# Kernel optimization log

Measured on AMD Instinct MI355X. Metric: run time of the kernel, lower is better.

The kernel has to match this reference:

```python
import jax, jax.numpy as jnp
import numpy as np

L, D, H, DFF, V, NB = 8, 1024, 16, 4096, 50257, 2048
HD = D // H
B, T = 2, 2048
EPS = 1e-5


def setup_inputs() -> dict:
    key = jax.random.key(0)
    ks = jax.random.split(key, 10)
    s = 0.02
    return {
        "x": jax.random.randint(ks[0], (B, T), 0, V),
        "W_emb": jax.random.normal(ks[1], (V, D), jnp.float32) * s,  # tied tok_emb / out_head
        "pos_emb": jax.random.normal(ks[2], (NB, D), jnp.float32) * s,
        "Wq": jax.random.normal(ks[3], (L, D, D), jnp.float32) * s,
        "Wk": jax.random.normal(ks[4], (L, D, D), jnp.float32) * s,
        "Wv": jax.random.normal(ks[5], (L, D, D), jnp.float32) * s,
        "Wo": jax.random.normal(ks[6], (L, D, D), jnp.float32) * s,
        "bo": jnp.zeros((L, D), jnp.float32),
        "n1_scale": jnp.ones((L, D), jnp.float32),
        "n1_shift": jnp.zeros((L, D), jnp.float32),
        "n2_scale": jnp.ones((L, D), jnp.float32),
        "n2_shift": jnp.zeros((L, D), jnp.float32),
        "W1": jax.random.normal(ks[7], (L, DFF, D), jnp.float32) * s,
        "b1": jnp.zeros((L, DFF), jnp.float32),
        "W2": jax.random.normal(ks[8], (L, D, DFF), jnp.float32) * s,
        "b2": jnp.zeros((L, D), jnp.float32),
        "f_scale": jnp.ones((D,), jnp.float32),
        "f_shift": jnp.zeros((D,), jnp.float32),
    }


def layernorm(x, scale, shift):
    # Matches custom LayerNorm: uses sample std (ddof=1) and (std + eps) in denominator
    mean = jnp.mean(x, axis=-1, keepdims=True)
    std = jnp.std(x, axis=-1, keepdims=True, ddof=1)
    return scale * ((x - mean) / (std + EPS)) + shift


def gelu(x):
    c = jnp.sqrt(jnp.asarray(2.0 / jnp.pi, x.dtype))
    return 0.5 * x * (1.0 + jnp.tanh(c * (x + 0.044715 * x * x * x)))


def reference(x, W_emb, pos_emb, Wq, Wk, Wv, Wo, bo,
              n1_scale, n1_shift, n2_scale, n2_shift,
              W1, b1, W2, b2, f_scale, f_shift):
    b, t = x.shape
    h = W_emb[x] + pos_emb[:t]  # [B,T,D]
    causal = jnp.triu(jnp.ones((t, t), dtype=bool), 1)  # True above diagonal => masked
    scale = jnp.sqrt(jnp.asarray(HD, h.dtype))
    neg_inf = jnp.asarray(-jnp.inf, h.dtype)
    for l in range(L):
        xn = layernorm(h, n1_scale[l], n1_shift[l])
        q = (xn @ Wq[l].T).reshape(b, t, H, HD).transpose(0, 2, 1, 3)  # [B,H,T,hd]
        k = (xn @ Wk[l].T).reshape(b, t, H, HD).transpose(0, 2, 1, 3)
        v = (xn @ Wv[l].T).reshape(b, t, H, HD).transpose(0, 2, 1, 3)
        scores = jnp.einsum('bhqd,bhkd->bhqk', q, k)
        scores = jnp.where(causal, neg_inf, scores) / scale  # mask then scale, as in source
        aw = jax.nn.softmax(scores, axis=-1)
        ctx = jnp.einsum('bhqk,bhkd->bhqd', aw, v)
        ctx = ctx.transpose(0, 2, 1, 3).reshape(b, t, D)
        h = h + (ctx @ Wo[l].T + bo[l])
        xn2 = layernorm(h, n2_scale[l], n2_shift[l])
        h = h + (gelu(xn2 @ W1[l].T + b1[l]) @ W2[l].T + b2[l])
    h = layernorm(h, f_scale, f_shift)
    logits = h[:, -1:, :] @ W_emb.T  # last-token logits [B,1,V] (targets=None path)
    return logits
```

## Files before the change

### kernel.cpp

```cpp
#include <hip/hip_runtime.h>
#include <math.h>

#define L_   8
#define D_   1024
#define H_   16
#define HD_  64
#define DFF_ 4096
#define V_   50257
#define T_   2048
#define B_   2
#define M_   (B_*T_)

typedef __attribute__((ext_vector_type(8))) short short8;
typedef __attribute__((ext_vector_type(4))) float f4;
typedef __attribute__((ext_vector_type(4))) unsigned short us4;

#define GLOAD16(gp, lp) \
  __builtin_amdgcn_global_load_lds((__attribute__((address_space(1))) void*)(gp), \
                                   (__attribute__((address_space(3))) void*)(lp), 16, 0, 0)

__device__ __forceinline__ unsigned short f2bf(float f) {
  union { float f; unsigned u; } c; c.f = f;
  return (unsigned short)((c.u + 0x7fffu + ((c.u >> 16) & 1u)) >> 16);
}

__global__ __launch_bounds__(256) void cvt_kernel(const float* __restrict__ s,
                                                  unsigned short* __restrict__ d, int n) {
  int i = (blockIdx.x * 256 + threadIdx.x) * 4;
  const int stride = gridDim.x * 256 * 4;
  for (; i < n; i += stride) {
    f4 f = *(const f4*)(s + i);
    us4 o;
    o.x = f2bf(f.x); o.y = f2bf(f.y); o.z = f2bf(f.z); o.w = f2bf(f.w);
    *(us4*)(d + i) = o;
  }
}

__global__ __launch_bounds__(256) void embed_kernel(const int* __restrict__ x,
    const float* __restrict__ wemb, const float* __restrict__ pos, float* __restrict__ h) {
  const int m = blockIdx.x;
  const int t = m & (T_ - 1);
  const int idx = x[m];
  const int d = threadIdx.x * 4;
  f4 a = *(const f4*)(wemb + (size_t)idx * D_ + d);
  f4 b = *(const f4*)(pos + (size_t)t * D_ + d);
  a = a + b;
  *(f4*)(h + (size_t)m * D_ + d) = a;
}

__global__ __launch_bounds__(256) void ln_kernel(const float* __restrict__ h,
    const float* __restrict__ sc, const float* __restrict__ sh,
    unsigned short* __restrict__ out) {
  const int row = blockIdx.x, tid = threadIdx.x;
  f4 x = *(const f4*)(h + (size_t)row * D_ + tid * 4);
  float s1 = x.x + x.y + x.z + x.w;
  float s2 = x.x * x.x + x.y * x.y + x.z * x.z + x.w * x.w;
#pragma unroll
  for (int off = 32; off > 0; off >>= 1) {
    s1 += __shfl_down(s1, off);
    s2 += __shfl_down(s2, off);
  }
  __shared__ float r1[4], r2[4];
  if ((tid & 63) == 0) { r1[tid >> 6] = s1; r2[tid >> 6] = s2; }
  __syncthreads();
  float t1 = r1[0] + r1[1] + r1[2] + r1[3];
  float t2 = r2[0] + r2[1] + r2[2] + r2[3];
  float mean = t1 * (1.0f / D_);
  float var = fmaxf((t2 - t1 * mean) * (1.0f / (D_ - 1)), 0.0f);
  float inv = 1.0f / (sqrtf(var) + 1e-5f);
  f4 s = *(const f4*)(sc + tid * 4);
  f4 b = *(const f4*)(sh + tid * 4);
  us4 o;
  o.x = f2bf(s.x * ((x.x - mean) * inv) + b.x);
  o.y = f2bf(s.y * ((x.y - mean) * inv) + b.y);
  o.z = f2bf(s.z * ((x.z - mean) * inv) + b.z);
  o.w = f2bf(s.w * ((x.w - mean) * inv) + b.w);
  *(us4*)(out + (size_t)row * D_ + tid * 4) = o;
}

__global__ __launch_bounds__(256) void ln_final_kernel(const float* __restrict__ h,
    const float* __restrict__ sc, const float* __restrict__ sh, float* __restrict__ out) {
  const int b = blockIdx.x, tid = threadIdx.x;
  const int row = b * T_ + (T_ - 1);
  f4 x = *(const f4*)(h + (size_t)row * D_ + tid * 4);
  float s1 = x.x + x.y + x.z + x.w;
  float s2 = x.x * x.x + x.y * x.y + x.z * x.z + x.w * x.w;
#pragma unroll
  for (int off = 32; off > 0; off >>= 1) {
    s1 += __shfl_down(s1, off);
    s2 += __shfl_down(s2, off);
  }
  __shared__ float r1[4], r2[4];
  if ((tid & 63) == 0) { r1[tid >> 6] = s1; r2[tid >> 6] = s2; }
  __syncthreads();
  float t1 = r1[0] + r1[1] + r1[2] + r1[3];
  float t2 = r2[0] + r2[1] + r2[2] + r2[3];
  float mean = t1 * (1.0f / D_);
  float var = fmaxf((t2 - t1 * mean) * (1.0f / (D_ - 1)), 0.0f);
  float inv = 1.0f / (sqrtf(var) + 1e-5f);
  f4 s = *(const f4*)(sc + tid * 4);
  f4 bb = *(const f4*)(sh + tid * 4);
  f4 o;
  o.x = s.x * ((x.x - mean) * inv) + bb.x;
  o.y = s.y * ((x.y - mean) * inv) + bb.y;
  o.z = s.z * ((x.z - mean) * inv) + bb.z;
  o.w = s.w * ((x.w - mean) * inv) + bb.w;
  *(f4*)(out + (size_t)b * D_ + tid * 4) = o;
}

#define EP_QKV 0
#define EP_RES 1
#define EP_GELU 2

template <int MODE>
__global__ __launch_bounds__(256) void gemm_kernel(
    const unsigned short* __restrict__ A,
    const unsigned short* __restrict__ Bq,
    const unsigned short* __restrict__ Bk,
    const unsigned short* __restrict__ Bv,
    const float* __restrict__ bias,
    float* __restrict__ hres,
    unsigned short* __restrict__ out0,
    unsigned short* __restrict__ out1,
    unsigned short* __restrict__ out2,
    int N, int K) {
  __shared__ __attribute__((aligned(16))) unsigned short As[128 * 32];
  __shared__ __attribute__((aligned(16))) unsigned short Bs[128 * 32];
  const int tid = threadIdx.x;
  const int wv = tid >> 6, lane = tid & 63;
  const int quad = lane >> 4, l16 = lane & 15;
  const int bm0 = blockIdx.x * 128;
  int bn0;
  const unsigned short* Bw;
  unsigned short* qout = out0;
  if (MODE == EP_QKV) {
    int sel = blockIdx.y >> 3;
    bn0 = (blockIdx.y & 7) * 128;
    Bw = (sel == 0) ? Bq : ((sel == 1) ? Bk : Bv);
    qout = (sel == 0) ? out0 : ((sel == 1) ? out1 : out2);
  } else {
    bn0 = blockIdx.y * 128;
    Bw = Bq;
  }
  const int wm = (wv & 1) * 64, wn = (wv >> 1) * 64;

  f4 acc[4][4] = {};

  for (int k0 = 0; k0 < K; k0 += 32) {
#pragma unroll
    for (int i = 0; i < 2; i++) {
      int c = i * 256 + tid;
      int row = c >> 2;
      int c4 = (c & 3) ^ (row & 3);
      GLOAD16(A + (size_t)(bm0 + row) * K + k0 + c4 * 8,
              (char*)As + (i * 256 + wv * 64) * 16);
      GLOAD16(Bw + (size_t)(bn0 + row) * K + k0 + c4 * 8,
              (char*)Bs + (i * 256 + wv * 64) * 16);
    }
    __syncthreads();
    short8 af[4], bfr[4];
#pragma unroll
    for (int mt = 0; mt < 4; mt++) {
      int row = wm + mt * 16 + l16;
      af[mt] = *(const short8*)(As + row * 32 + ((quad ^ (row & 3)) * 8));
    }
#pragma unroll
    for (int nt = 0; nt < 4; nt++) {
      int row = wn + nt * 16 + l16;
      bfr[nt] = *(const short8*)(Bs + row * 32 + ((quad ^ (row & 3)) * 8));
    }
#pragma unroll
    for (int mt = 0; mt < 4; mt++)
#pragma unroll
      for (int nt = 0; nt < 4; nt++)
        acc[mt][nt] = __builtin_amdgcn_mfma_f32_16x16x32_bf16(af[mt], bfr[nt], acc[mt][nt], 0, 0, 0);
    __syncthreads();
  }

#pragma unroll
  for (int mt = 0; mt < 4; mt++) {
#pragma unroll
    for (int nt = 0; nt < 4; nt++) {
#pragma unroll
      for (int r = 0; r < 4; r++) {
        int gm = bm0 + wm + mt * 16 + quad * 4 + r;
        int gn = bn0 + wn + nt * 16 + l16;
        float val = acc[mt][nt][r];
        if (MODE == EP_QKV) {
          int b = gm >> 11, t = gm & (T_ - 1);
          int hh = gn >> 6, hd = gn & 63;
          qout[(size_t)((b * H_ + hh) * T_ + t) * HD_ + hd] = f2bf(val);
        } else if (MODE == EP_RES) {
          size_t idx = (size_t)gm * D_ + gn;
          hres[idx] += val + bias[gn];
        } else {
          float xg = val + bias[gn];
          float z = 0.7978845608028654f * (xg + 0.044715f * xg * xg * xg);
          float e = __expf(2.0f * z);
          float th = 1.0f - 2.0f / (e + 1.0f);
          out0[(size_t)gm * DFF_ + gn] = f2bf(0.5f * xg * (1.0f + th));
        }
      }
    }
  }
}

__global__ __launch_bounds__(256) void vtrans_kernel(const unsigned short* __restrict__ v,
                                                     unsigned short* __restrict__ vt) {
  __shared__ __attribute__((aligned(16))) unsigned short tile[64 * 72];
  const int tid = threadIdx.x;
  const int t0 = blockIdx.x * 64;
  const size_t bh = (size_t)(blockIdx.z * H_ + blockIdx.y);
  const unsigned short* vp = v + bh * T_ * HD_;
#pragma unroll
  for (int i = 0; i < 2; i++) {
    int c = i * 256 + tid;
    int row = c >> 3, c8 = c & 7;
    *(short8*)(tile + row * 72 + c8 * 8) =
        *(const short8*)(vp + (size_t)(t0 + row) * HD_ + c8 * 8);
  }
  __syncthreads();
  unsigned short* op = vt + bh * (size_t)HD_ * T_;
#pragma unroll
  for (int i = 0; i < 2; i++) {
    int c = i * 256 + tid;
    int drow = c >> 3, c8 = c & 7;
    short8 o;
#pragma unroll
    for (int j = 0; j < 8; j++) o[j] = (short)tile[(c8 * 8 + j) * 72 + drow];
    *(short8*)(op + (size_t)drow * T_ + t0 + c8 * 8) = o;
  }
}

__global__ __launch_bounds__(256) void attn_kernel(
    const unsigned short* __restrict__ q,
    const unsigned short* __restrict__ k,
    const unsigned short* __restrict__ vt,
    unsigned short* __restrict__ ctx) {
  __shared__ __attribute__((aligned(16))) unsigned short Ks[64 * 64];
  __shared__ __attribute__((aligned(16))) unsigned short Vs[64 * 64];
  __shared__ __attribute__((aligned(16))) unsigned short Ps[4][16 * 88];
  const int tid = threadIdx.x;
  const int wv = tid >> 6, lane = tid & 63;
  const int quad = lane >> 4, l16 = lane & 15;
  const int qt = blockIdx.x, hh = blockIdx.y, b = blockIdx.z;
  const size_t bh = (size_t)(b * H_ + hh);
  const unsigned short* qp = q + bh * T_ * HD_;
  const unsigned short* kp = k + bh * T_ * HD_;
  const unsigned short* vp = vt + bh * (size_t)HD_ * T_;

  const int qrow = qt * 64 + wv * 16 + l16;
  const short8 qf0 = *(const short8*)(qp + (size_t)qrow * HD_ + quad * 8);
  const short8 qf1 = *(const short8*)(qp + (size_t)qrow * HD_ + 32 + quad * 8);

  f4 of[4] = {};
  float mrow[4] = {-1e30f, -1e30f, -1e30f, -1e30f};
  float lrow[4] = {0.f, 0.f, 0.f, 0.f};
  unsigned short* pw = Ps[wv];

  const int nkt = qt + 1;
  for (int kt = 0; kt < nkt; kt++) {
    const int kb = kt * 64;
#pragma unroll
    for (int i = 0; i < 2; i++) {
      int c = i * 256 + tid;
      int row = c >> 3;
      int c8 = (c & 7) ^ (row & 7);
      GLOAD16(kp + (size_t)(kb + row) * HD_ + c8 * 8, (char*)Ks + (i * 256 + wv * 64) * 16);
      GLOAD16(vp + (size_t)row * T_ + kb + c8 * 8, (char*)Vs + (i * 256 + wv * 64) * 16);
    }
    __syncthreads();
    float sv[4][4];
#pragma unroll
    for (int nt = 0; nt < 4; nt++) {
      int row = nt * 16 + l16;
      int p0 = (quad ^ (row & 7)) * 8;
      int p1 = ((4 + quad) ^ (row & 7)) * 8;
      short8 kf0 = *(const short8*)(Ks + row * 64 + p0);
      short8 kf1 = *(const short8*)(Ks + row * 64 + p1);
      f4 z = {};
      z = __builtin_amdgcn_mfma_f32_16x16x32_bf16(qf0, kf0, z, 0, 0, 0);
      z = __builtin_amdgcn_mfma_f32_16x16x32_bf16(qf1, kf1, z, 0, 0, 0);
#pragma unroll
      for (int r = 0; r < 4; r++) {
        float s = z[r] * 0.125f;
        if (kt == qt) {
          int col = kb + nt * 16 + l16;
          int rowg = qt * 64 + wv * 16 + quad * 4 + r;
          if (col > rowg) s = -1e30f;
        }
        sv[nt][r] = s;
      }
    }
    float mnew[4], alpha[4];
#pragma unroll
    for (int r = 0; r < 4; r++) {
      float mx = fmaxf(fmaxf(sv[0][r], sv[1][r]), fmaxf(sv[2][r], sv[3][r]));
      mx = fmaxf(mx, __shfl_xor(mx, 1));
      mx = fmaxf(mx, __shfl_xor(mx, 2));
      mx = fmaxf(mx, __shfl_xor(mx, 4));
      mx = fmaxf(mx, __shfl_xor(mx, 8));
      mnew[r] = fmaxf(mrow[r], mx);
      alpha[r] = __expf(mrow[r] - mnew[r]);
      mrow[r] = mnew[r];
    }
    float pv[4][4];
#pragma unroll
    for (int nt = 0; nt < 4; nt++)
#pragma unroll
      for (int r = 0; r < 4; r++)
        pv[nt][r] = __expf(sv[nt][r] - mnew[r]);
#pragma unroll
    for (int r = 0; r < 4; r++) {
      float s = pv[0][r] + pv[1][r] + pv[2][r] + pv[3][r];
      s += __shfl_xor(s, 1);
      s += __shfl_xor(s, 2);
      s += __shfl_xor(s, 4);
      s += __shfl_xor(s, 8);
      lrow[r] = lrow[r] * alpha[r] + s;
    }
#pragma unroll
    for (int nt = 0; nt < 4; nt++) {
      of[nt][0] *= alpha[0];
      of[nt][1] *= alpha[1];
      of[nt][2] *= alpha[2];
      of[nt][3] *= alpha[3];
    }
#pragma unroll
    for (int nt = 0; nt < 4; nt++)
#pragma unroll
      for (int r = 0; r < 4; r++)
        pw[(quad * 4 + r) * 88 + nt * 16 + l16] = f2bf(pv[nt][r]);
    short8 pf0 = *(const short8*)(pw + l16 * 88 + quad * 8);
    short8 pf1 = *(const short8*)(pw + l16 * 88 + 32 + quad * 8);
#pragma unroll
    for (int nt = 0; nt < 4; nt++) {
      int row = nt * 16 + l16;
      int p0 = (quad ^ (row & 7)) * 8;
      int p1 = ((4 + quad) ^ (row & 7)) * 8;
      short8 vf0 = *(const short8*)(Vs + row * 64 + p0);
      short8 vf1 = *(const short8*)(Vs + row * 64 + p1);
      of[nt] = __builtin_amdgcn_mfma_f32_16x16x32_bf16(pf0, vf0, of[nt], 0, 0, 0);
      of[nt] = __builtin_amdgcn_mfma_f32_16x16x32_bf16(pf1, vf1, of[nt], 0, 0, 0);
    }
    __syncthreads();
  }
#pragma unroll
  for (int nt = 0; nt < 4; nt++) {
#pragma unroll
    for (int r = 0; r < 4; r++) {
      int rowg = qt * 64 + wv * 16 + quad * 4 + r;
      int dcol = hh * HD_ + nt * 16 + l16;
      ctx[(size_t)(b * T_ + rowg) * D_ + dcol] = f2bf(of[nt][r] / lrow[r]);
    }
  }
}

__global__ __launch_bounds__(256) void logits_kernel(const float* __restrict__ wemb,
    const float* __restrict__ hln, float* __restrict__ out) {
  const int tid = threadIdx.x;
  const int wv = tid >> 6, lane = tid & 63;
  const int rbase = blockIdx.x * 32 + wv * 8;
  f4 h0[4], h1[4];
#pragma unroll
  for (int j = 0; j < 4; j++) {
    h0[j] = *(const f4*)(hln + j * 256 + lane * 4);
    h1[j] = *(const f4*)(hln + D_ + j * 256 + lane * 4);
  }
#pragma unroll
  for (int i = 0; i < 8; i++) {
    int r = rbase + i;
    if (r >= V_) return;
    const float* wr = wemb + (size_t)r * D_;
    float a0 = 0.f, a1 = 0.f;
#pragma unroll
    for (int j = 0; j < 4; j++) {
      f4 w4 = *(const f4*)(wr + j * 256 + lane * 4);
      a0 += w4.x * h0[j].x + w4.y * h0[j].y + w4.z * h0[j].z + w4.w * h0[j].w;
      a1 += w4.x * h1[j].x + w4.y * h1[j].y + w4.z * h1[j].z + w4.w * h1[j].w;
    }
#pragma unroll
    for (int off = 32; off > 0; off >>= 1) {
      a0 += __shfl_down(a0, off);
      a1 += __shfl_down(a1, off);
    }
    if (lane == 0) {
      out[r] = a0;
      out[V_ + r] = a1;
    }
  }
}

extern "C" void kernel_launch(void* const* d_in, const int* in_sizes, int n_in,
                              void* d_out, int out_size, void* d_ws, size_t ws_size,
                              hipStream_t stream) {
  (void)in_sizes; (void)n_in; (void)out_size; (void)ws_size;
  const int*   x    = (const int*)  d_in[0];
  const float* Wemb = (const float*)d_in[1];
  const float* pos  = (const float*)d_in[2];
  const float* Wq   = (const float*)d_in[3];
  const float* Wk   = (const float*)d_in[4];
  const float* Wv   = (const float*)d_in[5];
  const float* Wo   = (const float*)d_in[6];
  const float* bo   = (const float*)d_in[7];
  const float* n1s  = (const float*)d_in[8];
  const float* n1b  = (const float*)d_in[9];
  const float* n2s  = (const float*)d_in[10];
  const float* n2b  = (const float*)d_in[11];
  const float* W1   = (const float*)d_in[12];
  const float* b1   = (const float*)d_in[13];
  const float* W2   = (const float*)d_in[14];
  const float* b2   = (const float*)d_in[15];
  const float* fsc  = (const float*)d_in[16];
  const float* fsh  = (const float*)d_in[17];
  float* out = (float*)d_out;

  char* p = (char*)d_ws;
  auto alloc = [&](size_t bytes) -> char* {
    char* r = p;
    p += (bytes + 255) & ~(size_t)255;
    return r;
  };
  unsigned short* wq_b = (unsigned short*)alloc((size_t)L_ * D_ * D_ * 2);
  unsigned short* wk_b = (unsigned short*)alloc((size_t)L_ * D_ * D_ * 2);
  unsigned short* wv_b = (unsigned short*)alloc((size_t)L_ * D_ * D_ * 2);
  unsigned short* wo_b = (unsigned short*)alloc((size_t)L_ * D_ * D_ * 2);
  unsigned short* w1_b = (unsigned short*)alloc((size_t)L_ * DFF_ * D_ * 2);
  unsigned short* w2_b = (unsigned short*)alloc((size_t)L_ * DFF_ * D_ * 2);
  float*          h    = (float*)alloc((size_t)M_ * D_ * 4);
  unsigned short* xn   = (unsigned short*)alloc((size_t)M_ * D_ * 2);
  unsigned short* qb   = (unsigned short*)alloc((size_t)M_ * D_ * 2);
  unsigned short* kb   = (unsigned short*)alloc((size_t)M_ * D_ * 2);
  unsigned short* vb   = (unsigned short*)alloc((size_t)M_ * D_ * 2);
  unsigned short* vtb  = (unsigned short*)alloc((size_t)M_ * D_ * 2);
  unsigned short* ctx  = (unsigned short*)alloc((size_t)M_ * D_ * 2);
  unsigned short* act  = (unsigned short*)alloc((size_t)M_ * DFF_ * 2);
  float*          hln  = (float*)alloc(2 * D_ * 4);

  cvt_kernel<<<2048, 256, 0, stream>>>(Wq, wq_b, L_ * D_ * D_);
  cvt_kernel<<<2048, 256, 0, stream>>>(Wk, wk_b, L_ * D_ * D_);
  cvt_kernel<<<2048, 256, 0, stream>>>(Wv, wv_b, L_ * D_ * D_);
  cvt_kernel<<<2048, 256, 0, stream>>>(Wo, wo_b, L_ * D_ * D_);
  cvt_kernel<<<2048, 256, 0, stream>>>(W1, w1_b, L_ * DFF_ * D_);
  cvt_kernel<<<2048, 256, 0, stream>>>(W2, w2_b, L_ * DFF_ * D_);
  embed_kernel<<<M_, 256, 0, stream>>>(x, Wemb, pos, h);

  for (int l = 0; l < L_; l++) {
    ln_kernel<<<M_, 256, 0, stream>>>(h, n1s + l * D_, n1b + l * D_, xn);
    gemm_kernel<EP_QKV><<<dim3(32, 24), 256, 0, stream>>>(
        xn, wq_b + (size_t)l * D_ * D_, wk_b + (size_t)l * D_ * D_,
        wv_b + (size_t)l * D_ * D_, nullptr, nullptr, qb, kb, vb, D_, D_);
    vtrans_kernel<<<dim3(32, H_, B_), 256, 0, stream>>>(vb, vtb);
    attn_kernel<<<dim3(32, H_, B_), 256, 0, stream>>>(qb, kb, vtb, ctx);
    gemm_kernel<EP_RES><<<dim3(32, 8), 256, 0, stream>>>(
        ctx, wo_b + (size_t)l * D_ * D_, nullptr, nullptr,
        bo + l * D_, h, nullptr, nullptr, nullptr, D_, D_);
    ln_kernel<<<M_, 256, 0, stream>>>(h, n2s + l * D_, n2b + l * D_, xn);
    gemm_kernel<EP_GELU><<<dim3(32, 32), 256, 0, stream>>>(
        xn, w1_b + (size_t)l * DFF_ * D_, nullptr, nullptr,
        b1 + l * DFF_, nullptr, act, nullptr, nullptr, DFF_, D_);
    gemm_kernel<EP_RES><<<dim3(32, 8), 256, 0, stream>>>(
        act, w2_b + (size_t)l * DFF_ * D_, nullptr, nullptr,
        b2 + l * D_, h, nullptr, nullptr, nullptr, D_, DFF_);
  }
  ln_final_kernel<<<2, 256, 0, stream>>>(h, fsc, fsh, hln);
  logits_kernel<<<(V_ + 31) / 32, 256, 0, stream>>>(Wemb, hln, out);
}
```

Measured before the change: 3.668 ms.

## Pair complementary causal query tiles per attention block to balance work

Each attention block now processes two query tiles, bx and 31-bx, sharing the same K/V tile loads from shared memory, so every block does roughly equal causal work and loaded K/V tiles are reused by both. The grid is halved to 16 blocks in x, and launch bounds request two blocks per CU. This aims to remove tail imbalance from triangular causal work and cut redundant K/V loads. The cost is more registers for two sets of accumulators and fewer total blocks (512), which may reduce occupancy or latency hiding.

Measured after the change: 3.263 ms. -11.0%, faster.

```diff
diff --git a/kernel.cpp b/kernel.cpp
--- a/kernel.cpp
+++ b/kernel.cpp
@@ -232,7 +232,74 @@
   }
 }
 
-__global__ __launch_bounds__(256) void attn_kernel(
+#define ATTN_STEP(QF0, QF1, OF, MR, LR, QT)                                        \
+  {                                                                                \
+    float sv[4][4];                                                                \
+    _Pragma("unroll") for (int nt = 0; nt < 4; nt++) {                             \
+      int row = nt * 16 + l16;                                                     \
+      int p0 = (quad ^ (row & 7)) * 8;                                             \
+      int p1 = ((4 + quad) ^ (row & 7)) * 8;                                       \
+      short8 kf0 = *(const short8*)(Ks + row * 64 + p0);                           \
+      short8 kf1 = *(const short8*)(Ks + row * 64 + p1);                           \
+      f4 z = {};                                                                   \
+      z = __builtin_amdgcn_mfma_f32_16x16x32_bf16(QF0, kf0, z, 0, 0, 0);           \
+      z = __builtin_amdgcn_mfma_f32_16x16x32_bf16(QF1, kf1, z, 0, 0, 0);           \
+      _Pragma("unroll") for (int r = 0; r < 4; r++) {                              \
+        float s = z[r] * 0.125f;                                                   \
+        if (kt == (QT)) {                                                          \
+          int col = kb + nt * 16 + l16;                                            \
+          int rowg = (QT) * 64 + wv * 16 + quad * 4 + r;                           \
+          if (col > rowg) s = -1e30f;                                              \
+        }                                                                          \
+        sv[nt][r] = s;                                                             \
+      }                                                                            \
+    }                                                                              \
+    float mnew[4], alpha[4];                                                       \
+    _Pragma("unroll") for (int r = 0; r < 4; r++) {                                \
+      float mx = fmaxf(fmaxf(sv[0][r], sv[1][r]), fmaxf(sv[2][r], sv[3][r]));      \
+      mx = fmaxf(mx, __shfl_xor(mx, 1));                                           \
+      mx = fmaxf(mx, __shfl_xor(mx, 2));                                           \
+      mx = fmaxf(mx, __shfl_xor(mx, 4));                                           \
+      mx = fmaxf(mx, __shfl_xor(mx, 8));                                           \
+      mnew[r] = fmaxf(MR[r], mx);                                                  \
+      alpha[r] = __expf(MR[r] - mnew[r]);                                          \
+      MR[r] = mnew[r];                                                             \
+    }                                                                              \
+    float pv[4][4];                                                                \
+    _Pragma("unroll") for (int nt = 0; nt < 4; nt++)                               \
+      _Pragma("unroll") for (int r = 0; r < 4; r++)                                \
+        pv[nt][r] = __expf(sv[nt][r] - mnew[r]);                                   \
+    _Pragma("unroll") for (int r = 0; r < 4; r++) {                                \
+      float s = pv[0][r] + pv[1][r] + pv[2][r] + pv[3][r];                         \
+      s += __shfl_xor(s, 1);                                                       \
+      s += __shfl_xor(s, 2);                                                       \
+      s += __shfl_xor(s, 4);                                                       \
+      s += __shfl_xor(s, 8);                                                       \
+      LR[r] = LR[r] * alpha[r] + s;                                                \
+    }                                                                              \
+    _Pragma("unroll") for (int nt = 0; nt < 4; nt++) {                             \
+      OF[nt][0] *= alpha[0];                                                       \
+      OF[nt][1] *= alpha[1];                                                       \
+      OF[nt][2] *= alpha[2];                                                       \
+      OF[nt][3] *= alpha[3];                                                       \
+    }                                                                              \
+    _Pragma("unroll") for (int nt = 0; nt < 4; nt++)                               \
+      _Pragma("unroll") for (int r = 0; r < 4; r++)                                \
+        pw[(quad * 4 + r) * 88 + nt * 16 + l16] = f2bf(pv[nt][r]);                 \
+    short8 pf0 = *(const short8*)(pw + l16 * 88 + quad * 8);                       \
+    short8 pf1 = *(const short8*)(pw + l16 * 88 + 32 + quad * 8);                  \
+    _Pragma("unroll") for (int nt = 0; nt < 4; nt++) {                             \
+      int row = nt * 16 + l16;                                                     \
+      int p0 = (quad ^ (row & 7)) * 8;                                             \
+      int p1 = ((4 + quad) ^ (row & 7)) * 8;                                       \
+      short8 vf0 = *(const short8*)(Vs + row * 64 + p0);                           \
+      short8 vf1 = *(const short8*)(Vs + row * 64 + p1);                           \
+      OF[nt] = __builtin_amdgcn_mfma_f32_16x16x32_bf16(pf0, vf0, OF[nt], 0, 0, 0); \
+      OF[nt] = __builtin_amdgcn_mfma_f32_16x16x32_bf16(pf1, vf1, OF[nt], 0, 0, 0); \
+    }                                                                              \
+  }
+
+__global__ __launch_bounds__(256, 2) void attn_kernel(
     const unsigned short* __restrict__ q,
     const unsigned short* __restrict__ k,
     const unsigned short* __restrict__ vt,
@@ -243,22 +310,26 @@
   const int tid = threadIdx.x;
   const int wv = tid >> 6, lane = tid & 63;
   const int quad = lane >> 4, l16 = lane & 15;
-  const int qt = blockIdx.x, hh = blockIdx.y, b = blockIdx.z;
+  const int bx = blockIdx.x, hh = blockIdx.y, b = blockIdx.z;
+  const int qtA = bx, qtB = 31 - bx;
   const size_t bh = (size_t)(b * H_ + hh);
   const unsigned short* qp = q + bh * T_ * HD_;
   const unsigned short* kp = k + bh * T_ * HD_;
   const unsigned short* vp = vt + bh * (size_t)HD_ * T_;
 
-  const int qrow = qt * 64 + wv * 16 + l16;
-  const short8 qf0 = *(const short8*)(qp + (size_t)qrow * HD_ + quad * 8);
-  const short8 qf1 = *(const short8*)(qp + (size_t)qrow * HD_ + 32 + quad * 8);
-
-  f4 of[4] = {};
-  float mrow[4] = {-1e30f, -1e30f, -1e30f, -1e30f};
-  float lrow[4] = {0.f, 0.f, 0.f, 0.f};
+  const int qrA = qtA * 64 + wv * 16 + l16;
+  const int qrB = qtB * 64 + wv * 16 + l16;
+  const short8 qfA0 = *(const short8*)(qp + (size_t)qrA * HD_ + quad * 8);
+  const short8 qfA1 = *(const short8*)(qp + (size_t)qrA * HD_ + 32 + quad * 8);
+  const short8 qfB0 = *(const short8*)(qp + (size_t)qrB * HD_ + quad * 8);
+  const short8 qfB1 = *(const short8*)(qp + (size_t)qrB * HD_ + 32 + quad * 8);
+
+  f4 ofA[4] = {}, ofB[4] = {};
+  float mA[4] = {-1e30f, -1e30f, -1e30f, -1e30f}, lA[4] = {0.f, 0.f, 0.f, 0.f};
+  float mB[4] = {-1e30f, -1e30f, -1e30f, -1e30f}, lB[4] = {0.f, 0.f, 0.f, 0.f};
   unsigned short* pw = Ps[wv];
 
-  const int nkt = qt + 1;
+  const int nkt = qtB + 1;
   for (int kt = 0; kt < nkt; kt++) {
     const int kb = kt * 64;
 #pragma unroll
@@ -270,88 +341,19 @@
       GLOAD16(vp + (size_t)row * T_ + kb + c8 * 8, (char*)Vs + (i * 256 + wv * 64) * 16);
     }
     __syncthreads();
-    float sv[4][4];
-#pragma unroll
-    for (int nt = 0; nt < 4; nt++) {
-      int row = nt * 16 + l16;
-      int p0 = (quad ^ (row & 7)) * 8;
-      int p1 = ((4 + quad) ^ (row & 7)) * 8;
-      short8 kf0 = *(const short8*)(Ks + row * 64 + p0);
-      short8 kf1 = *(const short8*)(Ks + row * 64 + p1);
-      f4 z = {};
-      z = __builtin_amdgcn_mfma_f32_16x16x32_bf16(qf0, kf0, z, 0, 0, 0);
-      z = __builtin_amdgcn_mfma_f32_16x16x32_bf16(qf1, kf1, z, 0, 0, 0);
-#pragma unroll
-      for (int r = 0; r < 4; r++) {
-        float s = z[r] * 0.125f;
-        if (kt == qt) {
-          int col = kb + nt * 16 + l16;
-          int rowg = qt * 64 + wv * 16 + quad * 4 + r;
-          if (col > rowg) s = -1e30f;
-        }
-        sv[nt][r] = s;
-      }
-    }
-    float mnew[4], alpha[4];
+    ATTN_STEP(qfB0, qfB1, ofB, mB, lB, qtB);
+    if (kt <= qtA) ATTN_STEP(qfA0, qfA1, ofA, mA, lA, qtA);
+    __syncthreads();
+  }
+#pragma unroll
+  for (int nt = 0; nt < 4; nt++) {
 #pragma unroll
     for (int r = 0; r < 4; r++) {
-      float mx = fmaxf(fmaxf(sv[0][r], sv[1][r]), fmaxf(sv[2][r], sv[3][r]));
-      mx = fmaxf(mx, __shfl_xor(mx, 1));
-      mx = fmaxf(mx, __shfl_xor(mx, 2));
-      mx = fmaxf(mx, __shfl_xor(mx, 4));
-      mx = fmaxf(mx, __shfl_xor(mx, 8));
-      mnew[r] = fmaxf(mrow[r], mx);
-      alpha[r] = __expf(mrow[r] - mnew[r]);
-      mrow[r] = mnew[r];
-    }
-    float pv[4][4];
-#pragma unroll
-    for (int nt = 0; nt < 4; nt++)
-#pragma unroll
-      for (int r = 0; r < 4; r++)
-        pv[nt][r] = __expf(sv[nt][r] - mnew[r]);
-#pragma unroll
-    for (int r = 0; r < 4; r++) {
-      float s = pv[0][r] + pv[1][r] + pv[2][r] + pv[3][r];
-      s += __shfl_xor(s, 1);
-      s += __shfl_xor(s, 2);
-      s += __shfl_xor(s, 4);
-      s += __shfl_xor(s, 8);
-      lrow[r] = lrow[r] * alpha[r] + s;
-    }
-#pragma unroll
-    for (int nt = 0; nt < 4; nt++) {
-      of[nt][0] *= alpha[0];
-      of[nt][1] *= alpha[1];
-      of[nt][2] *= alpha[2];
-      of[nt][3] *= alpha[3];
-    }
-#pragma unroll
-    for (int nt = 0; nt < 4; nt++)
-#pragma unroll
-      for (int r = 0; r < 4; r++)
-        pw[(quad * 4 + r) * 88 + nt * 16 + l16] = f2bf(pv[nt][r]);
-    short8 pf0 = *(const short8*)(pw + l16 * 88 + quad * 8);
-    short8 pf1 = *(const short8*)(pw + l16 * 88 + 32 + quad * 8);
-#pragma unroll
-    for (int nt = 0; nt < 4; nt++) {
-      int row = nt * 16 + l16;
-      int p0 = (quad ^ (row & 7)) * 8;
-      int p1 = ((4 + quad) ^ (row & 7)) * 8;
-      short8 vf0 = *(const short8*)(Vs + row * 64 + p0);
-      short8 vf1 = *(const short8*)(Vs + row * 64 + p1);
-      of[nt] = __builtin_amdgcn_mfma_f32_16x16x32_bf16(pf0, vf0, of[nt], 0, 0, 0);
-      of[nt] = __builtin_amdgcn_mfma_f32_16x16x32_bf16(pf1, vf1, of[nt], 0, 0, 0);
-    }
-    __syncthreads();
-  }
-#pragma unroll
-  for (int nt = 0; nt < 4; nt++) {
-#pragma unroll
-    for (int r = 0; r < 4; r++) {
-      int rowg = qt * 64 + wv * 16 + quad * 4 + r;
       int dcol = hh * HD_ + nt * 16 + l16;
-      ctx[(size_t)(b * T_ + rowg) * D_ + dcol] = f2bf(of[nt][r] / lrow[r]);
+      int rowgB = qtB * 64 + wv * 16 + quad * 4 + r;
+      ctx[(size_t)(b * T_ + rowgB) * D_ + dcol] = f2bf(ofB[nt][r] / lB[r]);
+      int rowgA = qtA * 64 + wv * 16 + quad * 4 + r;
+      ctx[(size_t)(b * T_ + rowgA) * D_ + dcol] = f2bf(ofA[nt][r] / lA[r]);
     }
   }
 }
@@ -451,7 +453,7 @@
         xn, wq_b + (size_t)l * D_ * D_, wk_b + (size_t)l * D_ * D_,
         wv_b + (size_t)l * D_ * D_, nullptr, nullptr, qb, kb, vb, D_, D_);
     vtrans_kernel<<<dim3(32, H_, B_), 256, 0, stream>>>(vb, vtb);
-    attn_kernel<<<dim3(32, H_, B_), 256, 0, stream>>>(qb, kb, vtb, ctx);
+    attn_kernel<<<dim3(16, H_, B_), 256, 0, stream>>>(qb, kb, vtb, ctx);
     gemm_kernel<EP_RES><<<dim3(32, 8), 256, 0, stream>>>(
         ctx, wo_b + (size_t)l * D_ * D_, nullptr, nullptr,
         bo + l * D_, h, nullptr, nullptr, nullptr, D_, D_);
```
